# Kernel tuning notes

Measured on AMD Instinct MI355X. Metric: run time of the kernel, lower is better.

Reference implementation:

```python
import jax, jax.numpy as jnp
import numpy as np

ENTITY_ID_COL = 0  # EntityState 'id' attribute column
NUM_NPC_TYPES = 5
LN_EPS = 1e-5
NEG = -1e9


def layernorm(x, g, b):
    m = jnp.mean(x, axis=-1, keepdims=True)
    v = jnp.mean((x - m) ** 2, axis=-1, keepdims=True)
    return (x - m) * jax.lax.rsqrt(v + LN_EPS) * g + b


def gat_layer(x, mask, W, a_src, a_dst, ln_g, ln_b, num_heads, concat):
    B, N, _ = x.shape
    D = a_src.shape[-1]
    h = jnp.matmul(x, W).reshape(B, N, num_heads, D)          # [B,N,H,D]
    e_i = jnp.sum(h * a_src, axis=-1)                          # [B,N,H]
    e_j = jnp.sum(h * a_dst, axis=-1)                          # [B,N,H]
    # additive attention: e[b,i,j,h] = leakyrelu(e_i[b,i,h] + e_j[b,j,h])
    e = jax.nn.leaky_relu(e_i[:, :, None, :] + e_j[:, None, :, :], 0.2)
    mm = mask[:, :, None, None] * mask[:, None, :, None]       # [B,N,N,1]
    e = jnp.where(mm == 0, NEG, e)
    attn = jax.nn.softmax(e, axis=2)                           # softmax over j
    h_prime = jnp.einsum('bnjh,bjhd->bnhd', attn, h)
    if concat:
        h_prime = h_prime.reshape(B, N, num_heads * D)
    else:
        h_prime = h_prime.mean(axis=2)
    if h_prime.shape[-1] == x.shape[-1]:
        h_prime = layernorm(h_prime + x, ln_g, ln_b)
    else:
        h_prime = layernorm(h_prime, ln_g, ln_b)
    return h_prime


def setup_inputs() -> dict:
    key = jax.random.key(0)
    ks = jax.random.split(key, 12)
    B, N = 8, 1024
    entity_dim, hidden, heads, input_size = 31, 256, 4, 256
    d_head = hidden // heads  # 64
    merged_dim = entity_dim + 4  # 35 (npc_type expanded to 5 one-hot cols)

    agents = jax.random.normal(ks[0], (B, N, entity_dim), dtype=jnp.float32)
    npc_type = jax.random.randint(ks[1], (B, N), 0, NUM_NPC_TYPES).astype(jnp.float32)
    valid = (jax.random.uniform(ks[2], (B, N)) < 0.9).astype(jnp.float32)
    ids = jnp.arange(1, N + 1, dtype=jnp.float32)[None, :] * valid
    ids = ids.at[:, 0].set(1.0)  # guarantee id 1 exists in every batch row
    agents = agents.at[:, :, 0].set(ids)
    agents = agents.at[:, :, 1].set(npc_type)
    my_id = jnp.ones((B,), dtype=jnp.int32)

    def xavier(k, shape, fan_in, fan_out, gain=1.414):
        bound = gain * np.sqrt(6.0 / (fan_in + fan_out))
        return jax.random.uniform(k, shape, jnp.float32, -bound, bound)

    Wp = xavier(ks[3], (merged_dim, hidden), merged_dim, hidden, 1.0)
    bp = jnp.zeros((hidden,), jnp.float32)
    W1 = xavier(ks[4], (hidden, heads * d_head), hidden, heads * d_head)
    a_src1 = xavier(ks[5], (heads, d_head), heads, d_head)
    a_dst1 = xavier(ks[6], (heads, d_head), heads, d_head)
    ln1_g = jnp.ones((heads * d_head,), jnp.float32)
    ln1_b = jnp.zeros((heads * d_head,), jnp.float32)
    W2 = xavier(ks[7], (hidden, heads * d_head), hidden, heads * d_head)
    a_src2 = xavier(ks[8], (heads, d_head), heads, d_head)
    a_dst2 = xavier(ks[9], (heads, d_head), heads, d_head)
    ln2_g = jnp.ones((d_head,), jnp.float32)
    ln2_b = jnp.zeros((d_head,), jnp.float32)
    Wa = xavier(ks[10], (d_head, hidden), d_head, hidden, 1.0)
    ba = jnp.zeros((hidden,), jnp.float32)
    Wm = xavier(ks[11], (d_head, input_size), d_head, input_size, 1.0)
    bm = jnp.zeros((input_size,), jnp.float32)
    return dict(agents=agents, my_id=my_id, Wp=Wp, bp=bp,
                W1=W1, a_src1=a_src1, a_dst1=a_dst1, ln1_g=ln1_g, ln1_b=ln1_b,
                W2=W2, a_src2=a_src2, a_dst2=a_dst2, ln2_g=ln2_g, ln2_b=ln2_b,
                Wa=Wa, ba=ba, Wm=Wm, bm=bm)


def reference(agents, my_id, Wp, bp, W1, a_src1, a_dst1, ln1_g, ln1_b,
              W2, a_src2, a_dst2, ln2_g, ln2_b, Wa, ba, Wm, bm):
    num_heads = a_src1.shape[0]
    npc_type = agents[:, :, 1].astype(jnp.int32)
    one_hot = jax.nn.one_hot(npc_type, NUM_NPC_TYPES, dtype=jnp.float32)
    merged = jnp.concatenate([agents[:, :, :1], one_hot, agents[:, :, 2:]], axis=-1)
    mask = (merged[:, :, ENTITY_ID_COL] != 0).astype(jnp.float32)   # [B,N]
    proj = jnp.matmul(merged, Wp) + bp                              # [B,N,hidden]
    h1 = jax.nn.relu(gat_layer(proj, mask, W1, a_src1, a_dst1, ln1_g, ln1_b, num_heads, True))
    h2 = jax.nn.relu(gat_layer(h1, mask, W2, a_src2, a_dst2, ln2_g, ln2_b, num_heads, False))
    agent_embeddings = jnp.matmul(h2, Wa) + ba                      # [B,N,hidden]
    self_mask = merged[:, :, ENTITY_ID_COL] == my_id[:, None].astype(jnp.float32)
    idx = jnp.argmax(self_mask.astype(jnp.int32), axis=1)           # [B]
    my_emb = h2[jnp.arange(h2.shape[0]), idx]                       # [B,d_head]
    my_emb = jax.nn.relu(jnp.matmul(my_emb, Wm) + bm)
    return (agent_embeddings, my_emb)
```

## Files before the change

kernel.cpp:

```cpp
#include <hip/hip_runtime.h>
#include <hip/hip_bf16.h>

typedef _Float16 f16x8 __attribute__((ext_vector_type(8)));
typedef float f32x4 __attribute__((ext_vector_type(4)));

__global__ __launch_bounds__(256) void k_proj(
    const float* __restrict__ agents, const int* __restrict__ my_id,
    const float* __restrict__ Wp, const float* __restrict__ bp,
    float* __restrict__ proj, float* __restrict__ mask, int* __restrict__ idx)
{
  int blk = blockIdx.x;
  int b = blk >> 10, n = blk & 1023;
  __shared__ float arow[32];
  int t = threadIdx.x;
  if (t < 31) arow[t] = agents[((size_t)(b * 1024 + n)) * 31 + t];
  __syncthreads();
  float id = arow[0];
  int npc = (int)arow[1];
  float acc = bp[t] + id * Wp[t] + Wp[(1 + npc) * 256 + t];
#pragma unroll
  for (int c = 2; c < 31; ++c) acc += arow[c] * Wp[(4 + c) * 256 + t];
  proj[((size_t)(b * 1024 + n)) * 256 + t] = acc;
  if (t == 0) {
    mask[b * 1024 + n] = (id != 0.f) ? 1.f : 0.f;
    if (id == (float)my_id[b]) atomicMin(&idx[b], n);
  }
}

__global__ __launch_bounds__(256) void k_wt(
    const float* __restrict__ W, float* __restrict__ Wt, int K)
{
  __shared__ float tl[32][33];
  int bk = blockIdx.x >> 3, bj = blockIdx.x & 7;
  int tc = threadIdx.x & 31, tr = threadIdx.x >> 5;
#pragma unroll
  for (int r = 0; r < 4; ++r) {
    int row = tr * 4 + r;
    tl[row][tc] = W[(size_t)(bk * 32 + row) * 256 + bj * 32 + tc];
  }
  __syncthreads();
#pragma unroll
  for (int r = 0; r < 4; ++r) {
    int row = tr * 4 + r;
    Wt[(size_t)(bj * 32 + row) * K + bk * 32 + tc] = tl[tc][row];
  }
}

template <int K>
__global__ __launch_bounds__(256) void k_gemm_mfma(
    const float* __restrict__ A, const float* __restrict__ BtF,
    const float* __restrict__ bias, float* __restrict__ C)
{
  __shared__ __align__(16) _Float16 AsH[64 * 40], AsL[64 * 40];
  __shared__ __align__(16) _Float16 BsH[64 * 40], BsL[64 * 40];
  int t = threadIdx.x;
  int w = t >> 6, l = t & 63;
  int bi = blockIdx.x >> 2, bj = blockIdx.x & 3;
  int i0 = bi << 6, j0 = bj << 6;
  int srow = t >> 2, skq = (t & 3) << 3;

  f32x4 C0 = {0.f, 0.f, 0.f, 0.f}, C1 = C0, C2 = C0, C3 = C0;

  for (int k0 = 0; k0 < K; k0 += 32) {
    {
      const float* ap = A + (size_t)(i0 + srow) * K + k0 + skq;
      float4 a0 = *(const float4*)ap, a1 = *(const float4*)(ap + 4);
      float av[8] = {a0.x, a0.y, a0.z, a0.w, a1.x, a1.y, a1.z, a1.w};
      _Float16 hi[8], lo[8];
#pragma unroll
      for (int q = 0; q < 8; ++q) {
        hi[q] = (_Float16)av[q];
        lo[q] = (_Float16)(av[q] - (float)hi[q]);
      }
      *(uint4*)&AsH[srow * 40 + skq] = *(const uint4*)hi;
      *(uint4*)&AsL[srow * 40 + skq] = *(const uint4*)lo;
    }
    {
      const float* bp = BtF + (size_t)(j0 + srow) * K + k0 + skq;
      float4 b0 = *(const float4*)bp, b1 = *(const float4*)(bp + 4);
      float bv[8] = {b0.x, b0.y, b0.z, b0.w, b1.x, b1.y, b1.z, b1.w};
      _Float16 hi[8], lo[8];
#pragma unroll
      for (int q = 0; q < 8; ++q) {
        hi[q] = (_Float16)bv[q];
        lo[q] = (_Float16)(bv[q] - (float)hi[q]);
      }
      *(uint4*)&BsH[srow * 40 + skq] = *(const uint4*)hi;
      *(uint4*)&BsL[srow * 40 + skq] = *(const uint4*)lo;
    }
    __syncthreads();
    int fr = l & 15;
    int fk = (l >> 4) << 3;
    f16x8 ah = *(const f16x8*)&AsH[(w * 16 + fr) * 40 + fk];
    f16x8 al = *(const f16x8*)&AsL[(w * 16 + fr) * 40 + fk];
    {
      f16x8 bh = *(const f16x8*)&BsH[(0 * 16 + fr) * 40 + fk];
      f16x8 bl = *(const f16x8*)&BsL[(0 * 16 + fr) * 40 + fk];
      C0 = __builtin_amdgcn_mfma_f32_16x16x32_f16(ah, bh, C0, 0, 0, 0);
      C0 = __builtin_amdgcn_mfma_f32_16x16x32_f16(ah, bl, C0, 0, 0, 0);
      C0 = __builtin_amdgcn_mfma_f32_16x16x32_f16(al, bh, C0, 0, 0, 0);
    }
    {
      f16x8 bh = *(const f16x8*)&BsH[(1 * 16 + fr) * 40 + fk];
      f16x8 bl = *(const f16x8*)&BsL[(1 * 16 + fr) * 40 + fk];
      C1 = __builtin_amdgcn_mfma_f32_16x16x32_f16(ah, bh, C1, 0, 0, 0);
      C1 = __builtin_amdgcn_mfma_f32_16x16x32_f16(ah, bl, C1, 0, 0, 0);
      C1 = __builtin_amdgcn_mfma_f32_16x16x32_f16(al, bh, C1, 0, 0, 0);
    }
    {
      f16x8 bh = *(const f16x8*)&BsH[(2 * 16 + fr) * 40 + fk];
      f16x8 bl = *(const f16x8*)&BsL[(2 * 16 + fr) * 40 + fk];
      C2 = __builtin_amdgcn_mfma_f32_16x16x32_f16(ah, bh, C2, 0, 0, 0);
      C2 = __builtin_amdgcn_mfma_f32_16x16x32_f16(ah, bl, C2, 0, 0, 0);
      C2 = __builtin_amdgcn_mfma_f32_16x16x32_f16(al, bh, C2, 0, 0, 0);
    }
    {
      f16x8 bh = *(const f16x8*)&BsH[(3 * 16 + fr) * 40 + fk];
      f16x8 bl = *(const f16x8*)&BsL[(3 * 16 + fr) * 40 + fk];
      C3 = __builtin_amdgcn_mfma_f32_16x16x32_f16(ah, bh, C3, 0, 0, 0);
      C3 = __builtin_amdgcn_mfma_f32_16x16x32_f16(ah, bl, C3, 0, 0, 0);
      C3 = __builtin_amdgcn_mfma_f32_16x16x32_f16(al, bh, C3, 0, 0, 0);
    }
    __syncthreads();
  }

  int rbase = i0 + w * 16 + ((l >> 4) << 2);
  int cb = j0 + (l & 15);
  float b0 = bias ? bias[cb] : 0.f;
  float b1 = bias ? bias[cb + 16] : 0.f;
  float b2 = bias ? bias[cb + 32] : 0.f;
  float b3 = bias ? bias[cb + 48] : 0.f;
#pragma unroll
  for (int r = 0; r < 4; ++r) {
    size_t ro = (size_t)(rbase + r) * 256;
    C[ro + cb]      = C0[r] + b0;
    C[ro + cb + 16] = C1[r] + b1;
    C[ro + cb + 32] = C2[r] + b2;
    C[ro + cb + 48] = C3[r] + b3;
  }
}

__global__ __launch_bounds__(256) void k_edges(
    const float* __restrict__ h, const float* __restrict__ a_src,
    const float* __restrict__ a_dst, float* __restrict__ esrc, float* __restrict__ edst)
{
  __shared__ float as_[256], ad_[256];
  int t = threadIdx.x;
  as_[t] = a_src[t];
  ad_[t] = a_dst[t];
  __syncthreads();
  int w = t >> 6, l = t & 63;
  int row = blockIdx.x * 4 + w;
  const float* x = h + (size_t)row * 256;
  float ps[4], pd[4];
#pragma unroll
  for (int hh = 0; hh < 4; ++hh) {
    float v = x[hh * 64 + l];
    ps[hh] = v * as_[hh * 64 + l];
    pd[hh] = v * ad_[hh * 64 + l];
  }
#pragma unroll
  for (int hh = 0; hh < 4; ++hh) {
    for (int o = 32; o; o >>= 1) {
      ps[hh] += __shfl_down(ps[hh], o);
      pd[hh] += __shfl_down(pd[hh], o);
    }
  }
  if (l == 0) {
    int b = row >> 10, n = row & 1023;
#pragma unroll
    for (int hh = 0; hh < 4; ++hh) {
      esrc[((b * 4 + hh) << 10) + n] = ps[hh];
      edst[((b * 4 + hh) << 10) + n] = pd[hh];
    }
  }
}

__global__ __launch_bounds__(256) void k_emax(
    const float* __restrict__ edst, const float* __restrict__ mask, float* __restrict__ Mmax)
{
  int bh = blockIdx.x;
  int b = bh >> 2;
  int t = threadIdx.x;
  float v = -1e30f;
  for (int j = t; j < 1024; j += 256)
    if (mask[(b << 10) + j] != 0.f) v = fmaxf(v, edst[(bh << 10) + j]);
  for (int o = 32; o; o >>= 1) v = fmaxf(v, __shfl_down(v, o));
  __shared__ float red[4];
  if ((t & 63) == 0) red[t >> 6] = v;
  __syncthreads();
  if (t == 0) Mmax[bh] = fmaxf(fmaxf(red[0], red[1]), fmaxf(red[2], red[3]));
}

__global__ __launch_bounds__(256) void k_prep(
    const float* __restrict__ h, _Float16* __restrict__ hT)
{
  int blk = blockIdx.x;
  int c = blk & 31, hh = (blk >> 5) & 3, b = blk >> 7;
  int t = threadIdx.x;
  __shared__ _Float16 tile[32][72];
  {
    int jr = t >> 3, dg = t & 7;
    const float* src = h + ((size_t)(b * 1024 + c * 32 + jr)) * 256 + hh * 64 + dg * 8;
    float4 a = *(const float4*)src;
    float4 b4 = *(const float4*)(src + 4);
    _Float16* tp = &tile[jr][dg * 8];
    tp[0] = (_Float16)a.x;  tp[1] = (_Float16)a.y;  tp[2] = (_Float16)a.z;  tp[3] = (_Float16)a.w;
    tp[4] = (_Float16)b4.x; tp[5] = (_Float16)b4.y; tp[6] = (_Float16)b4.z; tp[7] = (_Float16)b4.w;
  }
  __syncthreads();
  {
    int d = t >> 2, q = t & 3;
    _Float16 o[8];
#pragma unroll
    for (int s = 0; s < 8; ++s) o[s] = tile[q * 8 + s][d];
    _Float16* dst = hT + ((size_t)((b * 4 + hh) * 32 + c)) * 2048 + d * 32 + q * 8;
    *(uint4*)dst = *(const uint4*)o;
  }
}

template <int LAYER>
__global__ __launch_bounds__(256) void k_attn_mfma(
    const _Float16* __restrict__ hT, const float* __restrict__ esrc,
    const float* __restrict__ edst, const float* __restrict__ Mmax,
    const float* __restrict__ mask, const float* __restrict__ resid,
    const float* __restrict__ g, const float* __restrict__ be,
    float* __restrict__ out)
{
  __shared__ __align__(16) char smem[40960];
  __shared__ float esrcL[16][4], mL[16][4];
  __shared__ float maskL[16], MhL[4];
  __shared__ float sInvS[4][16];
  __shared__ float statM[16], statR[16];

  int t = threadIdx.x;
  int hID = t >> 6, l = t & 63;
  int b = blockIdx.x & 7;
  int it = blockIdx.x >> 3;
  int i0 = it << 4;

  if (t < 16) maskL[t] = mask[(b << 10) + i0 + t];
  if (t < 4) MhL[t] = Mmax[(b << 2) + t];
  if (t < 64) {
    int ii = t >> 2, hh = t & 3;
    esrcL[ii][hh] = esrc[(((b << 2) + hh) << 10) + i0 + ii];
  }
  __syncthreads();
  if (t < 64) {
    int ii = t >> 2, hh = t & 3;
    float m = 0.f;
    if (maskL[ii] != 0.f) {
      float v = esrcL[ii][hh] + MhL[hh];
      m = v > 0.f ? v : 0.2f * v;
    }
    mL[ii][hh] = m;
  }
  __syncthreads();

  int iloc = l & 15;
  float esr = esrcL[iloc][hID];
  float mr = mL[iloc][hID];
  float mskI = maskL[iloc];
  int jg = (l >> 4) << 3;

  const float* ej_base = edst + (((b << 2) + hID) << 10);
  const float* mk_base = mask + (b << 10);
  const char* gT = (const char*)hT + ((size_t)((b * 4 + hID) * 32)) * 4096;
  char* hb = smem + hID * 10240;

  f32x4 C0 = {0.f,0.f,0.f,0.f}, C1 = C0, C2 = C0, C3 = C0;
  float sp = 0.f;

  {
    const uint4* gs = (const uint4*)(gT + l * 64);
    uint4 s0 = gs[0], s1 = gs[1], s2 = gs[2], s3 = gs[3];
    uint4* wp = (uint4*)(hb + l * 80);
    wp[0] = s0; wp[1] = s1; wp[2] = s2; wp[3] = s3;
  }
  int cur = 0;

  for (int c = 0; c < 32; ++c) {
    uint4 n0, n1, n2, n3;
    if (c < 31) {
      const uint4* gs = (const uint4*)(gT + (size_t)(c + 1) * 4096 + l * 64);
      n0 = gs[0]; n1 = gs[1]; n2 = gs[2]; n3 = gs[3];
    }
    int j0 = c << 5;
    float4 e0 = *(const float4*)(ej_base + j0 + jg);
    float4 e1 = *(const float4*)(ej_base + j0 + jg + 4);
    float4 m0 = *(const float4*)(mk_base + j0 + jg);
    float4 m1 = *(const float4*)(mk_base + j0 + jg + 4);
    float w[8];
    float ev[8] = {e0.x, e0.y, e0.z, e0.w, e1.x, e1.y, e1.z, e1.w};
    float mv[8] = {m0.x, m0.y, m0.z, m0.w, m1.x, m1.y, m1.z, m1.w};
    if (mskI != 0.f) {
#pragma unroll
      for (int q = 0; q < 8; ++q) {
        float v = esr + ev[q];
        v = v > 0.f ? v : 0.2f * v;
        w[q] = (mv[q] != 0.f) ? __expf(v - mr) : 0.f;
      }
    } else {
#pragma unroll
      for (int q = 0; q < 8; ++q) w[q] = 1.f;
    }
    f16x8 af;
#pragma unroll
    for (int q = 0; q < 8; ++q) { sp += w[q]; af[q] = (_Float16)w[q]; }
    const char* rp = hb + cur * 5120 + (l & 15) * 80 + (l >> 4) * 16;
    f16x8 b0 = *(const f16x8*)(rp);
    f16x8 b1 = *(const f16x8*)(rp + 1280);
    f16x8 b2 = *(const f16x8*)(rp + 2560);
    f16x8 b3 = *(const f16x8*)(rp + 3840);
    C0 = __builtin_amdgcn_mfma_f32_16x16x32_f16(af, b0, C0, 0, 0, 0);
    C1 = __builtin_amdgcn_mfma_f32_16x16x32_f16(af, b1, C1, 0, 0, 0);
    C2 = __builtin_amdgcn_mfma_f32_16x16x32_f16(af, b2, C2, 0, 0, 0);
    C3 = __builtin_amdgcn_mfma_f32_16x16x32_f16(af, b3, C3, 0, 0, 0);
    if (c < 31) {
      uint4* wp = (uint4*)(hb + (cur ^ 1) * 5120 + l * 80);
      wp[0] = n0; wp[1] = n1; wp[2] = n2; wp[3] = n3;
      cur ^= 1;
    }
  }

  sp += __shfl_xor(sp, 16);
  sp += __shfl_xor(sp, 32);
  if (l < 16) sInvS[hID][l] = 1.f / sp;
  __syncthreads();

  float (*y)[256] = (float (*)[256])smem;
  {
    int rbase = (l >> 4) << 2;
    int col = (hID << 6) + (l & 15);
#pragma unroll
    for (int r = 0; r < 4; ++r) {
      float sv = sInvS[hID][rbase + r];
      y[rbase + r][col +  0] = C0[r] * sv;
      y[rbase + r][col + 16] = C1[r] * sv;
      y[rbase + r][col + 32] = C2[r] * sv;
      y[rbase + r][col + 48] = C3[r] * sv;
    }
  }
  __syncthreads();

  if (LAYER == 1) {
#pragma unroll
    for (int i = 0; i < 16; ++i)
      y[i][t] += resid[((size_t)(b * 1024 + i0 + i)) * 256 + t];
    __syncthreads();
#pragma unroll
    for (int rr = 0; rr < 4; ++rr) {
      int i = (hID << 2) + rr;
      float v0 = y[i][l], v1 = y[i][64 + l], v2 = y[i][128 + l], v3 = y[i][192 + l];
      float s = v0 + v1 + v2 + v3;
      float q = v0 * v0 + v1 * v1 + v2 * v2 + v3 * v3;
      for (int o = 32; o; o >>= 1) { s += __shfl_xor(s, o); q += __shfl_xor(q, o); }
      if (l == 0) {
        float mean = s * (1.f / 256.f);
        float var = q * (1.f / 256.f) - mean * mean;
        statM[i] = mean;
        statR[i] = rsqrtf(var + 1e-5f);
      }
    }
    __syncthreads();
#pragma unroll
    for (int i = 0; i < 16; ++i) {
      float yv = y[i][t];
      float o_ = (yv - statM[i]) * statR[i] * g[t] + be[t];
      out[((size_t)(b * 1024 + i0 + i)) * 256 + t] = fmaxf(o_, 0.f);
    }
  } else {
#pragma unroll
    for (int rr = 0; rr < 4; ++rr) {
      int i = (hID << 2) + rr;
      float v = 0.25f * (y[i][l] + y[i][64 + l] + y[i][128 + l] + y[i][192 + l]);
      float s = v, q = v * v;
      for (int o = 32; o; o >>= 1) { s += __shfl_xor(s, o); q += __shfl_xor(q, o); }
      float mean = s * (1.f / 64.f);
      float var = q * (1.f / 64.f) - mean * mean;
      float rstd = rsqrtf(var + 1e-5f);
      float o_ = (v - mean) * rstd * g[l] + be[l];
      out[((size_t)(b * 1024 + i0 + i)) * 64 + l] = fmaxf(o_, 0.f);
    }
  }
}

__global__ __launch_bounds__(256) void k_myemb(
    const float* __restrict__ h2, const int* __restrict__ idx,
    const float* __restrict__ Wm, const float* __restrict__ bm, float* __restrict__ out)
{
  __shared__ float row[64];
  int t = threadIdx.x;
  for (int b = 0; b < 8; ++b) {
    int n = idx[b];
    if (t < 64) row[t] = h2[((size_t)(b * 1024 + n)) * 64 + t];
    __syncthreads();
    float acc = bm[t];
#pragma unroll
    for (int d = 0; d < 64; ++d) acc += row[d] * Wm[d * 256 + t];
    out[2097152 + b * 256 + t] = fmaxf(acc, 0.f);
    __syncthreads();
  }
}

extern "C" void kernel_launch(void* const* d_in, const int* in_sizes, int n_in,
                              void* d_out, int out_size, void* d_ws, size_t ws_size,
                              hipStream_t stream) {
  const float* agents = (const float*)d_in[0];
  const int* my_id = (const int*)d_in[1];
  const float* Wp = (const float*)d_in[2];
  const float* bp = (const float*)d_in[3];
  const float* W1 = (const float*)d_in[4];
  const float* a_src1 = (const float*)d_in[5];
  const float* a_dst1 = (const float*)d_in[6];
  const float* ln1_g = (const float*)d_in[7];
  const float* ln1_b = (const float*)d_in[8];
  const float* W2 = (const float*)d_in[9];
  const float* a_src2 = (const float*)d_in[10];
  const float* a_dst2 = (const float*)d_in[11];
  const float* ln2_g = (const float*)d_in[12];
  const float* ln2_b = (const float*)d_in[13];
  const float* Wa = (const float*)d_in[14];
  const float* ba = (const float*)d_in[15];
  const float* Wm = (const float*)d_in[16];
  const float* bm = (const float*)d_in[17];
  float* out = (float*)d_out;

  float* W = (float*)d_ws;
  float* mask = W;
  float* Mmax = W + 8192;
  int* idx = (int*)(W + 8224);
  float* esrc = W + 16384;
  float* edst = W + 49152;
  float* proj = W + 81920;
  float* htmp = W + 2179072;
  float* h1 = W + 4276224;
  float* h2 = W + 6373376;
  _Float16* hT = (_Float16*)(W + 6897664);
  float* Wt1 = W + 7946240;
  float* Wt2 = W + 8011776;
  float* Wta = W + 8077312;

  hipMemsetAsync(idx, 0x7F, 8 * sizeof(int), stream);
  k_proj<<<8192, 256, 0, stream>>>(agents, my_id, Wp, bp, proj, mask, idx);
  k_wt<<<64, 256, 0, stream>>>(W1, Wt1, 256);
  k_wt<<<64, 256, 0, stream>>>(W2, Wt2, 256);
  k_wt<<<16, 256, 0, stream>>>(Wa, Wta, 64);

  k_gemm_mfma<256><<<512, 256, 0, stream>>>(proj, Wt1, nullptr, htmp);
  k_prep<<<1024, 256, 0, stream>>>(htmp, hT);
  k_edges<<<2048, 256, 0, stream>>>(htmp, a_src1, a_dst1, esrc, edst);
  k_emax<<<32, 256, 0, stream>>>(edst, mask, Mmax);
  k_attn_mfma<1><<<512, 256, 0, stream>>>(hT, esrc, edst, Mmax, mask, proj, ln1_g, ln1_b, h1);

  k_gemm_mfma<256><<<512, 256, 0, stream>>>(h1, Wt2, nullptr, htmp);
  k_prep<<<1024, 256, 0, stream>>>(htmp, hT);
  k_edges<<<2048, 256, 0, stream>>>(htmp, a_src2, a_dst2, esrc, edst);
  k_emax<<<32, 256, 0, stream>>>(edst, mask, Mmax);
  k_attn_mfma<2><<<512, 256, 0, stream>>>(hT, esrc, edst, Mmax, mask, nullptr, ln2_g, ln2_b, h2);

  k_gemm_mfma<64><<<512, 256, 0, stream>>>(h2, Wta, ba, out);
  k_myemb<<<1, 256, 0, stream>>>(h2, idx, Wm, bm, out);
}
```

Measured before the change: 235.8 us.

## Fuse transpose into GEMM epilogue, merge edge/max kernels, batch weight transposes

The GEMM epilogue now writes the fp16 transposed per-head tile (hT) directly from its accumulators through shared memory, which removes the separate k_prep pass. The edge-score and masked-max kernels become a single k_edgemax kernel with one block per (batch, head). The three weight-transpose launches are merged into one. This cuts launches and one read of htmp per layer, but k_edgemax runs only 32 blocks, so its loop over nodes has low parallelism and could become a serial bottleneck.

```diff
diff --git a/kernel.cpp b/kernel.cpp
--- a/kernel.cpp
+++ b/kernel.cpp
@@ -27,11 +27,20 @@
   }
 }
 
-__global__ __launch_bounds__(256) void k_wt(
-    const float* __restrict__ W, float* __restrict__ Wt, int K)
+__global__ __launch_bounds__(256) void k_wt_all(
+    const float* __restrict__ W1, const float* __restrict__ W2,
+    const float* __restrict__ Wa, float* __restrict__ Wt1,
+    float* __restrict__ Wt2, float* __restrict__ Wta)
 {
   __shared__ float tl[32][33];
-  int bk = blockIdx.x >> 3, bj = blockIdx.x & 7;
+  int blk = blockIdx.x;
+  const float* W;
+  float* Wt;
+  int K;
+  if (blk < 64)      { W = W1; Wt = Wt1; K = 256; }
+  else if (blk < 128){ W = W2; Wt = Wt2; K = 256; blk -= 64; }
+  else               { W = Wa; Wt = Wta; K = 64;  blk -= 128; }
+  int bk = blk >> 3, bj = blk & 7;
   int tc = threadIdx.x & 31, tr = threadIdx.x >> 5;
 #pragma unroll
   for (int r = 0; r < 4; ++r) {
@@ -46,13 +55,15 @@
   }
 }
 
-template <int K>
+template <int K, bool WRITE_HT>
 __global__ __launch_bounds__(256) void k_gemm_mfma(
     const float* __restrict__ A, const float* __restrict__ BtF,
-    const float* __restrict__ bias, float* __restrict__ C)
+    const float* __restrict__ bias, float* __restrict__ C,
+    _Float16* __restrict__ hT)
 {
   __shared__ __align__(16) _Float16 AsH[64 * 40], AsL[64 * 40];
   __shared__ __align__(16) _Float16 BsH[64 * 40], BsL[64 * 40];
+  __shared__ __align__(16) _Float16 tile[64][72];
   int t = threadIdx.x;
   int w = t >> 6, l = t & 63;
   int bi = blockIdx.x >> 2, bj = blockIdx.x & 3;
@@ -138,85 +149,64 @@
     C[ro + cb + 32] = C2[r] + b2;
     C[ro + cb + 48] = C3[r] + b3;
   }
-}
-
-__global__ __launch_bounds__(256) void k_edges(
+
+  if (WRITE_HT) {
+    int jl = w * 16 + ((l >> 4) << 2);
+    int d0 = l & 15;
+#pragma unroll
+    for (int r = 0; r < 4; ++r) {
+      tile[d0][jl + r]      = (_Float16)C0[r];
+      tile[d0 + 16][jl + r] = (_Float16)C1[r];
+      tile[d0 + 32][jl + r] = (_Float16)C2[r];
+      tile[d0 + 48][jl + r] = (_Float16)C3[r];
+    }
+    __syncthreads();
+    int d = t >> 2, cc = (t >> 1) & 1, gg = t & 1;
+    int bb = bi >> 4;
+    int c = ((bi & 15) << 1) + cc;
+    _Float16* dst = hT + ((size_t)((bb * 4 + bj) * 32 + c)) * 2048 + d * 32 + gg * 16;
+    const _Float16* srcp = &tile[d][cc * 32 + gg * 16];
+    ((uint4*)dst)[0] = ((const uint4*)srcp)[0];
+    ((uint4*)dst)[1] = ((const uint4*)srcp)[1];
+  }
+}
+
+__global__ __launch_bounds__(256) void k_edgemax(
     const float* __restrict__ h, const float* __restrict__ a_src,
-    const float* __restrict__ a_dst, float* __restrict__ esrc, float* __restrict__ edst)
-{
-  __shared__ float as_[256], ad_[256];
+    const float* __restrict__ a_dst, const float* __restrict__ mask,
+    float* __restrict__ esrc, float* __restrict__ edst, float* __restrict__ Mmax)
+{
+  int bh = blockIdx.x;
+  int b = bh >> 2, hh = bh & 3;
   int t = threadIdx.x;
-  as_[t] = a_src[t];
-  ad_[t] = a_dst[t];
-  __syncthreads();
   int w = t >> 6, l = t & 63;
-  int row = blockIdx.x * 4 + w;
-  const float* x = h + (size_t)row * 256;
-  float ps[4], pd[4];
-#pragma unroll
-  for (int hh = 0; hh < 4; ++hh) {
-    float v = x[hh * 64 + l];
-    ps[hh] = v * as_[hh * 64 + l];
-    pd[hh] = v * ad_[hh * 64 + l];
-  }
-#pragma unroll
-  for (int hh = 0; hh < 4; ++hh) {
-    for (int o = 32; o; o >>= 1) {
-      ps[hh] += __shfl_down(ps[hh], o);
-      pd[hh] += __shfl_down(pd[hh], o);
-    }
-  }
-  if (l == 0) {
-    int b = row >> 10, n = row & 1023;
-#pragma unroll
-    for (int hh = 0; hh < 4; ++hh) {
-      esrc[((b * 4 + hh) << 10) + n] = ps[hh];
-      edst[((b * 4 + hh) << 10) + n] = pd[hh];
-    }
-  }
-}
-
-__global__ __launch_bounds__(256) void k_emax(
-    const float* __restrict__ edst, const float* __restrict__ mask, float* __restrict__ Mmax)
-{
-  int bh = blockIdx.x;
-  int b = bh >> 2;
-  int t = threadIdx.x;
-  float v = -1e30f;
-  for (int j = t; j < 1024; j += 256)
-    if (mask[(b << 10) + j] != 0.f) v = fmaxf(v, edst[(bh << 10) + j]);
-  for (int o = 32; o; o >>= 1) v = fmaxf(v, __shfl_down(v, o));
+  int dq = (l & 15) << 2;
+  int rloc = l >> 4;
+  float4 as4 = *(const float4*)(a_src + hh * 64 + dq);
+  float4 ad4 = *(const float4*)(a_dst + hh * 64 + dq);
+  float mmax = -1e30f;
+  for (int it = 0; it < 64; ++it) {
+    int j = (w << 8) + (it << 2) + rloc;
+    float4 hv = *(const float4*)(h + ((size_t)(b * 1024 + j)) * 256 + hh * 64 + dq);
+    float ps = hv.x * as4.x + hv.y * as4.y + hv.z * as4.z + hv.w * as4.w;
+    float pd = hv.x * ad4.x + hv.y * ad4.y + hv.z * ad4.z + hv.w * ad4.w;
+#pragma unroll
+    for (int o = 1; o < 16; o <<= 1) {
+      ps += __shfl_xor(ps, o);
+      pd += __shfl_xor(pd, o);
+    }
+    if ((l & 15) == 0) {
+      esrc[(bh << 10) + j] = ps;
+      edst[(bh << 10) + j] = pd;
+    }
+    if (mask[(b << 10) + j] != 0.f) mmax = fmaxf(mmax, pd);
+  }
+  mmax = fmaxf(mmax, __shfl_xor(mmax, 16));
+  mmax = fmaxf(mmax, __shfl_xor(mmax, 32));
   __shared__ float red[4];
-  if ((t & 63) == 0) red[t >> 6] = v;
+  if (l == 0) red[w] = mmax;
   __syncthreads();
   if (t == 0) Mmax[bh] = fmaxf(fmaxf(red[0], red[1]), fmaxf(red[2], red[3]));
-}
-
-__global__ __launch_bounds__(256) void k_prep(
-    const float* __restrict__ h, _Float16* __restrict__ hT)
-{
-  int blk = blockIdx.x;
-  int c = blk & 31, hh = (blk >> 5) & 3, b = blk >> 7;
-  int t = threadIdx.x;
-  __shared__ _Float16 tile[32][72];
-  {
-    int jr = t >> 3, dg = t & 7;
-    const float* src = h + ((size_t)(b * 1024 + c * 32 + jr)) * 256 + hh * 64 + dg * 8;
-    float4 a = *(const float4*)src;
-    float4 b4 = *(const float4*)(src + 4);
-    _Float16* tp = &tile[jr][dg * 8];
-    tp[0] = (_Float16)a.x;  tp[1] = (_Float16)a.y;  tp[2] = (_Float16)a.z;  tp[3] = (_Float16)a.w;
-    tp[4] = (_Float16)b4.x; tp[5] = (_Float16)b4.y; tp[6] = (_Float16)b4.z; tp[7] = (_Float16)b4.w;
-  }
-  __syncthreads();
-  {
-    int d = t >> 2, q = t & 3;
-    _Float16 o[8];
-#pragma unroll
-    for (int s = 0; s < 8; ++s) o[s] = tile[q * 8 + s][d];
-    _Float16* dst = hT + ((size_t)((b * 4 + hh) * 32 + c)) * 2048 + d * 32 + q * 8;
-    *(uint4*)dst = *(const uint4*)o;
-  }
 }
 
 template <int LAYER>
@@ -443,22 +433,16 @@
 
   hipMemsetAsync(idx, 0x7F, 8 * sizeof(int), stream);
   k_proj<<<8192, 256, 0, stream>>>(agents, my_id, Wp, bp, proj, mask, idx);
-  k_wt<<<64, 256, 0, stream>>>(W1, Wt1, 256);
-  k_wt<<<64, 256, 0, stream>>>(W2, Wt2, 256);
-  k_wt<<<16, 256, 0, stream>>>(Wa, Wta, 64);
-
-  k_gemm_mfma<256><<<512, 256, 0, stream>>>(proj, Wt1, nullptr, htmp);
-  k_prep<<<1024, 256, 0, stream>>>(htmp, hT);
-  k_edges<<<2048, 256, 0, stream>>>(htmp, a_src1, a_dst1, esrc, edst);
-  k_emax<<<32, 256, 0, stream>>>(edst, mask, Mmax);
+  k_wt_all<<<144, 256, 0, stream>>>(W1, W2, Wa, Wt1, Wt2, Wta);
+
+  k_gemm_mfma<256, true><<<512, 256, 0, stream>>>(proj, Wt1, nullptr, htmp, hT);
+  k_edgemax<<<32, 256, 0, stream>>>(htmp, a_src1, a_dst1, mask, esrc, edst, Mmax);
   k_attn_mfma<1><<<512, 256, 0, stream>>>(hT, esrc, edst, Mmax, mask, proj, ln1_g, ln1_b, h1);
 
-  k_gemm_mfma<256><<<512, 256, 0, stream>>>(h1, Wt2, nullptr, htmp);
-  k_prep<<<1024, 256, 0, stream>>>(htmp, hT);
-  k_edges<<<2048, 256, 0, stream>>>(htmp, a_src2, a_dst2, esrc, edst);
-  k_emax<<<32, 256, 0, stream>>>(edst, mask, Mmax);
+  k_gemm_mfma<256, true><<<512, 256, 0, stream>>>(h1, Wt2, nullptr, htmp, hT);
+  k_edgemax<<<32, 256, 0, stream>>>(htmp, a_src2, a_dst2, mask, esrc, edst, Mmax);
   k_attn_mfma<2><<<512, 256, 0, stream>>>(hT, esrc, edst, Mmax, mask, nullptr, ln2_g, ln2_b, h2);
 
-  k_gemm_mfma<64><<<512, 256, 0, stream>>>(h2, Wta, ba, out);
+  k_gemm_mfma<64, false><<<512, 256, 0, stream>>>(h2, Wta, ba, out, nullptr);
   k_myemb<<<1, 256, 0, stream>>>(h2, idx, Wm, bm, out);
 }
```

New measurement: 275.8 us. 17.0% more time.
